# Performance work log

Hardware: AMD Instinct MI355X
Metric: run time of the kernel (lower is better)

Reference implementation:

```python
import jax, jax.numpy as jnp
import numpy as np

NUM_EXPERTS = 32
TOP_K = 4
HIDDEN = 2048
INTER = 768


def setup_inputs() -> dict:
    key = jax.random.key(0)
    k1, k2, k3, k4 = jax.random.split(key, 4)
    hidden_states = jax.random.normal(k1, (4, 512, HIDDEN), dtype=jnp.float32)
    gate = jax.random.normal(k2, (HIDDEN, NUM_EXPERTS), dtype=jnp.float32) * 0.02
    gate_up_proj = jax.random.normal(k3, (NUM_EXPERTS, HIDDEN, 2 * INTER), dtype=jnp.float32) * 0.02
    down_proj = jax.random.normal(k4, (NUM_EXPERTS, INTER, HIDDEN), dtype=jnp.float32) * 0.02
    return {"hidden_states": hidden_states, "gate": gate,
            "gate_up_proj": gate_up_proj, "down_proj": down_proj}


def reference(hidden_states, gate, gate_up_proj, down_proj):
    batch_size = hidden_states.shape[0]
    x = hidden_states.reshape(-1, HIDDEN)  # (T, D)
    num_tokens = x.shape[0]

    # Router
    router_logits = jnp.einsum('TD,DE->TE', x, gate)
    routing_weights = jax.nn.softmax(router_logits.astype(jnp.float32), axis=-1)
    top_k_weights, top_k_indices = jax.lax.top_k(routing_weights, TOP_K)
    top_k_weights = top_k_weights / top_k_weights.sum(axis=-1, keepdims=True)
    top_k_weights = top_k_weights.astype(x.dtype)

    # Scatter top-k weights into full (T, E) matrix
    router_weights = jnp.zeros((num_tokens, NUM_EXPERTS), dtype=x.dtype)
    token_indices = jnp.broadcast_to(jnp.arange(num_tokens)[:, None], top_k_indices.shape)
    router_weights = router_weights.at[token_indices, top_k_indices].set(top_k_weights)

    # Dense all-expert experts pass (faithful to original: computes every expert per token)
    gate_up = jnp.einsum('TD,EDF->TEF', x, gate_up_proj)  # (T, E, 2F)
    g, u = jnp.split(gate_up, 2, axis=-1)
    gated = u * jax.nn.silu(g)  # (T, E, F)
    next_states = jnp.einsum('TEF,EFD->TED', gated, down_proj)
    next_states = (next_states * router_weights[..., None]).sum(axis=1)  # (T, D)
    return next_states.reshape(batch_size, -1, HIDDEN)
```

## Files before the change

kernel.cpp:

```cpp
#include <hip/hip_runtime.h>

#define T_TOKENS 2048
#define HIDDEN   2048
#define NEXPERT  32
#define TOPK     4
#define INTER    768
#define NPAIRS   (T_TOKENS*TOPK)
#define BM       128
#define BK       32
#define MT_MAX   95
#define NT1      24
#define NT2      32
#define NK1      (HIDDEN/BK)
#define NK2      (INTER/BK)

typedef short  bh8 __attribute__((ext_vector_type(8)));
typedef float  fx4 __attribute__((ext_vector_type(4)));

#define AS1 __attribute__((address_space(1)))
#define AS3 __attribute__((address_space(3)))

__device__ __forceinline__ void gload_lds16(const void* g, const void* lds_generic){
    __builtin_amdgcn_global_load_lds(
        (const AS1 void*)(unsigned long long)g,
        (AS3 void*)(unsigned int)(unsigned long long)lds_generic,
        16, 0, 0);
}

__device__ __forceinline__ unsigned int pack2bf(float a, float b){
    unsigned ua = __float_as_uint(a) + 0x8000u;
    unsigned ub = __float_as_uint(b) + 0x8000u;
    return __builtin_amdgcn_perm(ub, ua, 0x07060302u);
}
__device__ __forceinline__ unsigned short f2bfu(float f){
    return (unsigned short)((__float_as_uint(f) + 0x8000u) >> 16);
}

__global__ void cvt_x_k(const float* __restrict__ x, unsigned short* __restrict__ xb){
    int i = (blockIdx.x*256 + threadIdx.x)*8;
    float4 a = *(const float4*)(x+i);
    float4 b = *(const float4*)(x+i+4);
    uint4 o;
    o.x = pack2bf(a.x,a.y); o.y = pack2bf(a.z,a.w);
    o.z = pack2bf(b.x,b.y); o.w = pack2bf(b.z,b.w);
    *(uint4*)(xb+i) = o;
}

__global__ void router_k(const float* __restrict__ x, const float* __restrict__ gate,
                         int* __restrict__ topk_id, float* __restrict__ topk_w,
                         int* __restrict__ counts){
    const int t = blockIdx.x;
    const int l = threadIdx.x;
    const float* xr = x + (size_t)t*HIDDEN;
    float acc[NEXPERT];
#pragma unroll
    for (int e=0;e<NEXPERT;e++) acc[e]=0.f;
    for (int d=l; d<HIDDEN; d+=64){
        float xv = xr[d];
        const float4* g4 = (const float4*)(gate + (size_t)d*NEXPERT);
#pragma unroll
        for (int i=0;i<8;i++){
            float4 g = g4[i];
            acc[i*4+0] += xv*g.x; acc[i*4+1] += xv*g.y;
            acc[i*4+2] += xv*g.z; acc[i*4+3] += xv*g.w;
        }
    }
#pragma unroll
    for (int e=0;e<NEXPERT;e++){
#pragma unroll
        for (int m=1;m<64;m<<=1) acc[e] += __shfl_xor(acc[e], m, 64);
    }
    int ids[TOPK]; float lv[TOPK];
#pragma unroll
    for (int k=0;k<TOPK;k++){
        float m=-1e30f; int mi=0;
#pragma unroll
        for (int e=0;e<NEXPERT;e++){ if (acc[e]>m){ m=acc[e]; mi=e; } }
        ids[k]=mi; lv[k]=m; acc[mi]=-1e30f;
    }
    float ex[TOPK]; float s=0.f;
#pragma unroll
    for (int k=0;k<TOPK;k++){ ex[k]=__expf(lv[k]-lv[0]); s+=ex[k]; }
    if (l==0){
        float inv = 1.f/s;
#pragma unroll
        for (int k=0;k<TOPK;k++){
            topk_id[t*TOPK+k]=ids[k];
            topk_w[t*TOPK+k]=ex[k]*inv;
            atomicAdd(&counts[ids[k]],1);
        }
    }
}

__global__ void sched_k(const int* __restrict__ counts, int* __restrict__ offs,
                        int* __restrict__ cursors, int* __restrict__ nmt,
                        int* __restrict__ te, int* __restrict__ tr0, int* __restrict__ trn){
    if (threadIdx.x==0 && blockIdx.x==0){
        int tot=0, nm=0;
        for (int e=0;e<NEXPERT;e++){
            int c = counts[e];
            offs[e]=tot; cursors[e]=tot;
            for (int s=0;s<c;s+=BM){
                te[nm]=e; tr0[nm]=tot+s; trn[nm]=(c-s)<BM?(c-s):BM; nm++;
            }
            tot+=c;
        }
        *nmt = nm;
    }
}

__global__ void scatter_k(const int* __restrict__ topk_id, const float* __restrict__ topk_w,
                          int* __restrict__ cursors, int* __restrict__ pair_tok,
                          float* __restrict__ pair_w){
    int g = blockIdx.x*256 + threadIdx.x;
    int e = topk_id[g];
    float w = topk_w[g];
    int pos = atomicAdd(&cursors[e],1);
    pair_tok[pos] = g>>2;
    pair_w[pos]  = w;
}

#define TILE_DECODE(NT)                                            \
    const int nwg = gridDim.x;                                     \
    const int q = nwg>>3, r = nwg&7;                               \
    const int xcd = blockIdx.x & 7, bidx = blockIdx.x >> 3;        \
    const int L = (xcd<r ? xcd*(q+1) : r*(q+1)+(xcd-r)*q) + bidx;  \
    const int mt = L % MT_MAX, nt = L / MT_MAX;                    \
    if (mt >= *nmt) return;                                        \
    const int e = te[mt], row0 = tr0[mt], rows = trn[mt];

__global__ __launch_bounds__(256) void gemm1_k(
        const unsigned short* __restrict__ xb, const float* __restrict__ gup,
        const int* __restrict__ nmt, const int* __restrict__ te,
        const int* __restrict__ tr0, const int* __restrict__ trn,
        const int* __restrict__ pair_tok, const float* __restrict__ pair_w,
        unsigned short* __restrict__ gated){
    __shared__ __align__(16) unsigned short As[2][BM*32];
    __shared__ __align__(16) unsigned short Bs[2][64*40];
    __shared__ int   s_tok[BM];
    __shared__ float s_w[BM];

    TILE_DECODE(NT1)
    const int n0 = nt*32;

    const int t = threadIdx.x;
    if (t < BM){
        int p = row0 + t; if (p > NPAIRS-1) p = NPAIRS-1;
        s_tok[t] = pair_tok[p];
        s_w[t]   = pair_w[p];
    }
    __syncthreads();

    const int w = t>>6, lane = t&63;
    const int l15 = lane & 15, kb = lane >> 4;
    const int sA = (l15>>1)&3;

    const int arow0 = w*16 + (lane>>2);
    const int arow1 = 64 + arow0;
    const int ck0 = (lane&3) ^ ((lane>>3)&3);
    const unsigned short* asrc0 = xb + (size_t)s_tok[arow0]*HIDDEN + ck0*8;
    const unsigned short* asrc1 = xb + (size_t)s_tok[arow1]*HIDDEN + ck0*8;

    const int col4 = (t&15)*4;
    const int bd0  = (t>>4)*2;
    const int sB   = (col4>>3)&3;
    const unsigned wb = (unsigned)(col4*80 + (((bd0>>3) ^ sB)<<4) + (bd0&7)*2);
    const int fc = (col4 < 32) ? (n0 + col4) : (736 + n0 + col4);
    const float* bsrc = gup + (size_t)e*HIDDEN*(2*INTER) + (size_t)bd0*(2*INTER) + fc;

    fx4 acc[2][4];
#pragma unroll
    for (int i=0;i<2;i++)
#pragma unroll
        for (int j=0;j<4;j++) acc[i][j] = (fx4)0.f;

    float4 rv0 = *(const float4*)(bsrc);
    float4 rv1 = *(const float4*)(bsrc + 2*INTER);
    gload_lds16(asrc0, &As[0][(w*16)*32]);
    gload_lds16(asrc1, &As[0][(64+w*16)*32]);
    __syncthreads();
    {
        char* bw = (char*)Bs[0];
        *(unsigned*)(bw + wb      ) = pack2bf(rv0.x, rv1.x);
        *(unsigned*)(bw + wb +  80) = pack2bf(rv0.y, rv1.y);
        *(unsigned*)(bw + wb + 160) = pack2bf(rv0.z, rv1.z);
        *(unsigned*)(bw + wb + 240) = pack2bf(rv0.w, rv1.w);
    }
    __syncthreads();

#define G1_STEP(KK, CUR, NXT) do{                                              \
    const int _kn = (KK)+1;                                                    \
    if (_kn < NK1){                                                            \
        const float* _b2 = bsrc + (size_t)_kn*BK*(2*INTER);                    \
        rv0 = *(const float4*)(_b2);                                           \
        rv1 = *(const float4*)(_b2 + 2*INTER);                                 \
        gload_lds16(asrc0 + _kn*BK, &As[NXT][(w*16)*32]);                      \
        gload_lds16(asrc1 + _kn*BK, &As[NXT][(64+w*16)*32]);                   \
    }                                                                          \
    {   const unsigned short* _Ak = As[CUR];                                   \
        const char* _Bk = (const char*)Bs[CUR];                                \
        bh8 _a0 = *(const bh8*)(_Ak + (w*32+l15)*32    + ((kb ^ sA)<<3));      \
        bh8 _a1 = *(const bh8*)(_Ak + (w*32+16+l15)*32 + ((kb ^ sA)<<3));      \
        _Pragma("unroll")                                                      \
        for (int c=0;c<4;c++){                                                 \
            const int bc = c*16 + l15;                                         \
            bh8 _b = *(const bh8*)(_Bk + bc*80 + ((kb ^ ((bc>>3)&3))<<4));     \
            acc[0][c] = __builtin_amdgcn_mfma_f32_16x16x32_bf16(_a0,_b,acc[0][c],0,0,0); \
            acc[1][c] = __builtin_amdgcn_mfma_f32_16x16x32_bf16(_a1,_b,acc[1][c],0,0,0); \
        }                                                                      \
    }                                                                          \
    if (_kn < NK1){                                                            \
        char* _bw = (char*)Bs[NXT];                                            \
        *(unsigned*)(_bw + wb      ) = pack2bf(rv0.x, rv1.x);                  \
        *(unsigned*)(_bw + wb +  80) = pack2bf(rv0.y, rv1.y);                  \
        *(unsigned*)(_bw + wb + 160) = pack2bf(rv0.z, rv1.z);                  \
        *(unsigned*)(_bw + wb + 240) = pack2bf(rv0.w, rv1.w);                  \
    }                                                                          \
    __syncthreads();                                                           \
}while(0)

    for (int k2=0; k2<NK1; k2+=2){
        G1_STEP(k2,   0, 1);
        G1_STEP(k2+1, 1, 0);
    }
#undef G1_STEP

    const int rbase = w*32 + kb*4;
#pragma unroll
    for (int mr=0;mr<2;mr++){
#pragma unroll
        for (int qq=0;qq<4;qq++){
            int row = rbase + mr*16 + qq;
            if (row < rows){
                float wgt = s_w[row];
                size_t prow = (size_t)(row0 + row)*INTER + n0 + l15;
#pragma unroll
                for (int c=0;c<2;c++){
                    float g = acc[mr][c][qq], u = acc[mr][c+2][qq];
                    float sil = g / (1.f + __expf(-g));
                    gated[prow + c*16] = f2bfu(sil*u*wgt);
                }
            }
        }
    }
}

__global__ __launch_bounds__(256) void gemm2_k(
        const unsigned short* __restrict__ gated, const float* __restrict__ down,
        const int* __restrict__ nmt, const int* __restrict__ te,
        const int* __restrict__ tr0, const int* __restrict__ trn,
        const int* __restrict__ pair_tok, float* __restrict__ out){
    __shared__ __align__(16) unsigned short As[2][BM*32];
    __shared__ __align__(16) unsigned short Bs[2][64*40];
    __shared__ int s_tok[BM];

    TILE_DECODE(NT2)
    const int n0 = nt*64;

    const int t = threadIdx.x;
    if (t < BM){
        int p = row0 + t; if (p > NPAIRS-1) p = NPAIRS-1;
        s_tok[t] = pair_tok[p];
    }
    __syncthreads();

    const int w = t>>6, lane = t&63;
    const int l15 = lane & 15, kb = lane >> 4;
    const int sA = (l15>>1)&3;

    const int arow0 = w*16 + (lane>>2);
    const int arow1 = 64 + arow0;
    const int ck0 = (lane&3) ^ ((lane>>3)&3);
    int ap0 = row0 + arow0; if (ap0 > NPAIRS-1) ap0 = NPAIRS-1;
    int ap1 = row0 + arow1; if (ap1 > NPAIRS-1) ap1 = NPAIRS-1;
    const unsigned short* asrc0 = gated + (size_t)ap0*INTER + ck0*8;
    const unsigned short* asrc1 = gated + (size_t)ap1*INTER + ck0*8;

    const int col4 = (t&15)*4;
    const int bd0  = (t>>4)*2;
    const int sB   = (col4>>3)&3;
    const unsigned wb = (unsigned)(col4*80 + (((bd0>>3) ^ sB)<<4) + (bd0&7)*2);
    const float* bsrc = down + (size_t)e*INTER*HIDDEN + (size_t)bd0*HIDDEN + (n0 + col4);

    fx4 acc[2][4];
#pragma unroll
    for (int i=0;i<2;i++)
#pragma unroll
        for (int j=0;j<4;j++) acc[i][j] = (fx4)0.f;

    float4 rv0 = *(const float4*)(bsrc);
    float4 rv1 = *(const float4*)(bsrc + HIDDEN);
    gload_lds16(asrc0, &As[0][(w*16)*32]);
    gload_lds16(asrc1, &As[0][(64+w*16)*32]);
    __syncthreads();
    {
        char* bw = (char*)Bs[0];
        *(unsigned*)(bw + wb      ) = pack2bf(rv0.x, rv1.x);
        *(unsigned*)(bw + wb +  80) = pack2bf(rv0.y, rv1.y);
        *(unsigned*)(bw + wb + 160) = pack2bf(rv0.z, rv1.z);
        *(unsigned*)(bw + wb + 240) = pack2bf(rv0.w, rv1.w);
    }
    __syncthreads();

#define G2_STEP(KK, CUR, NXT) do{                                              \
    const int _kn = (KK)+1;                                                    \
    if (_kn < NK2){                                                            \
        const float* _b2 = bsrc + (size_t)_kn*BK*HIDDEN;                       \
        rv0 = *(const float4*)(_b2);                                           \
        rv1 = *(const float4*)(_b2 + HIDDEN);                                  \
        gload_lds16(asrc0 + _kn*BK, &As[NXT][(w*16)*32]);                      \
        gload_lds16(asrc1 + _kn*BK, &As[NXT][(64+w*16)*32]);                   \
    }                                                                          \
    {   const unsigned short* _Ak = As[CUR];                                   \
        const char* _Bk = (const char*)Bs[CUR];                                \
        bh8 _a0 = *(const bh8*)(_Ak + (w*32+l15)*32    + ((kb ^ sA)<<3));      \
        bh8 _a1 = *(const bh8*)(_Ak + (w*32+16+l15)*32 + ((kb ^ sA)<<3));      \
        _Pragma("unroll")                                                      \
        for (int c=0;c<4;c++){                                                 \
            const int bc = c*16 + l15;                                         \
            bh8 _b = *(const bh8*)(_Bk + bc*80 + ((kb ^ ((bc>>3)&3))<<4));     \
            acc[0][c] = __builtin_amdgcn_mfma_f32_16x16x32_bf16(_a0,_b,acc[0][c],0,0,0); \
            acc[1][c] = __builtin_amdgcn_mfma_f32_16x16x32_bf16(_a1,_b,acc[1][c],0,0,0); \
        }                                                                      \
    }                                                                          \
    if (_kn < NK2){                                                            \
        char* _bw = (char*)Bs[NXT];                                            \
        *(unsigned*)(_bw + wb      ) = pack2bf(rv0.x, rv1.x);                  \
        *(unsigned*)(_bw + wb +  80) = pack2bf(rv0.y, rv1.y);                  \
        *(unsigned*)(_bw + wb + 160) = pack2bf(rv0.z, rv1.z);                  \
        *(unsigned*)(_bw + wb + 240) = pack2bf(rv0.w, rv1.w);                  \
    }                                                                          \
    __syncthreads();                                                           \
}while(0)

    for (int k2=0; k2<NK2; k2+=2){
        G2_STEP(k2,   0, 1);
        G2_STEP(k2+1, 1, 0);
    }
#undef G2_STEP

    const int rbase = w*32 + kb*4;
#pragma unroll
    for (int mr=0;mr<2;mr++){
#pragma unroll
        for (int qq=0;qq<4;qq++){
            int row = rbase + mr*16 + qq;
            if (row < rows){
                float* orow = out + (size_t)s_tok[row]*HIDDEN + n0 + l15;
#pragma unroll
                for (int c=0;c<4;c++)
                    atomicAdd(orow + c*16, acc[mr][c][qq]);
            }
        }
    }
}

extern "C" void kernel_launch(void* const* d_in, const int* in_sizes, int n_in,
                              void* d_out, int out_size, void* d_ws, size_t ws_size,
                              hipStream_t stream){
    const float* x    = (const float*)d_in[0];
    const float* gate = (const float*)d_in[1];
    const float* gup  = (const float*)d_in[2];
    const float* down = (const float*)d_in[3];
    float* out = (float*)d_out;
    char*  ws  = (char*)d_ws;

    int*   topk_id  = (int*)  (ws + 0x00000);
    float* topk_w   = (float*)(ws + 0x08000);
    int*   counts   = (int*)  (ws + 0x10000);
    int*   cursors  = (int*)  (ws + 0x10080);
    int*   offs     = (int*)  (ws + 0x10100);
    int*   nmt      = (int*)  (ws + 0x10180);
    int*   te       = (int*)  (ws + 0x10200);
    int*   tr0      = (int*)  (ws + 0x10400);
    int*   trn      = (int*)  (ws + 0x10600);
    int*   pair_tok = (int*)  (ws + 0x10800);
    float* pair_w   = (float*)(ws + 0x18800);
    unsigned short* gated = (unsigned short*)(ws + 0x21000);
    unsigned short* xb    = (unsigned short*)(ws + 0xC60000);

    hipMemsetAsync(d_out, 0, (size_t)out_size*sizeof(float), stream);
    hipMemsetAsync(counts, 0, NEXPERT*sizeof(int), stream);

    cvt_x_k  <<<T_TOKENS*HIDDEN/(256*8), 256, 0, stream>>>(x, xb);
    router_k <<<T_TOKENS, 64, 0, stream>>>(x, gate, topk_id, topk_w, counts);
    sched_k  <<<1, 64, 0, stream>>>(counts, offs, cursors, nmt, te, tr0, trn);
    scatter_k<<<NPAIRS/256, 256, 0, stream>>>(topk_id, topk_w, cursors, pair_tok, pair_w);
    gemm1_k  <<<MT_MAX*NT1, 256, 0, stream>>>(xb, gup, nmt, te, tr0, trn, pair_tok, pair_w, gated);
    gemm2_k  <<<MT_MAX*NT2, 256, 0, stream>>>(gated, down, nmt, te, tr0, trn, pair_tok, out);
}
```

Baseline: 471.6 us.

## Triple-buffer LDS with prefetch distance two and partial vmcnt waits in both GEMMs

Both expert GEMM kernels move from a double-buffered LDS pipeline to a three-stage ring. The A tile (global_load_lds) and the B registers are prefetched two K-steps ahead, and the full __syncthreads is replaced by explicit s_waitcnt vmcnt(4)/lgkmcnt(0) plus s_barrier. The aim is to hide global load latency behind MFMA work and to stop waiting on loads that are still in flight. It costs 50% more LDS per block, which may lower occupancy. The hand-counted vmcnt values are fragile, and clamping the prefetch index at the tail issues redundant loads.

```diff
diff --git a/kernel.cpp b/kernel.cpp
--- a/kernel.cpp
+++ b/kernel.cpp
@@ -129,14 +129,44 @@
     if (mt >= *nmt) return;                                        \
     const int e = te[mt], row0 = tr0[mt], rows = trn[mt];
 
+#define GSTEP(KK, NK, BSTR, C0, C1, C2, RL0, RL1, RW0, RW1) do{                 \
+    int _ks = (KK)+2; if (_ks > (NK)-1) _ks = (NK)-1;                           \
+    const float* _bp = bsrc + (size_t)_ks*BK*(BSTR);                            \
+    RL0 = *(const float4*)(_bp);                                                \
+    RL1 = *(const float4*)(_bp + (BSTR));                                       \
+    gload_lds16(asrc0 + _ks*BK, &As[C2][(w*16)*32]);                            \
+    gload_lds16(asrc1 + _ks*BK, &As[C2][(64+w*16)*32]);                         \
+    {   const unsigned short* _Ak = As[C0];                                     \
+        const char* _Bk = (const char*)Bs[C0];                                  \
+        bh8 _a0 = *(const bh8*)(_Ak + (w*32+l15)*32    + ((kb^sA)<<3));         \
+        bh8 _a1 = *(const bh8*)(_Ak + (w*32+16+l15)*32 + ((kb^sA)<<3));         \
+        _Pragma("unroll")                                                       \
+        for (int c=0;c<4;c++){                                                  \
+            const int bc = c*16 + l15;                                          \
+            bh8 _b = *(const bh8*)(_Bk + bc*80 + ((kb ^ ((bc>>3)&3))<<4));      \
+            acc[0][c] = __builtin_amdgcn_mfma_f32_16x16x32_bf16(_a0,_b,acc[0][c],0,0,0); \
+            acc[1][c] = __builtin_amdgcn_mfma_f32_16x16x32_bf16(_a1,_b,acc[1][c],0,0,0); \
+        }                                                                       \
+    }                                                                           \
+    asm volatile("s_waitcnt vmcnt(4)" ::: "memory");                            \
+    {   char* _bw = (char*)Bs[C1];                                              \
+        *(unsigned*)(_bw + wb      ) = pack2bf(RW0.x, RW1.x);                   \
+        *(unsigned*)(_bw + wb +  80) = pack2bf(RW0.y, RW1.y);                   \
+        *(unsigned*)(_bw + wb + 160) = pack2bf(RW0.z, RW1.z);                   \
+        *(unsigned*)(_bw + wb + 240) = pack2bf(RW0.w, RW1.w);                   \
+    }                                                                           \
+    asm volatile("s_waitcnt lgkmcnt(0)" ::: "memory");                          \
+    __builtin_amdgcn_s_barrier();                                               \
+}while(0)
+
 __global__ __launch_bounds__(256) void gemm1_k(
         const unsigned short* __restrict__ xb, const float* __restrict__ gup,
         const int* __restrict__ nmt, const int* __restrict__ te,
         const int* __restrict__ tr0, const int* __restrict__ trn,
         const int* __restrict__ pair_tok, const float* __restrict__ pair_w,
         unsigned short* __restrict__ gated){
-    __shared__ __align__(16) unsigned short As[2][BM*32];
-    __shared__ __align__(16) unsigned short Bs[2][64*40];
+    __shared__ __align__(16) unsigned short As[3][BM*32];
+    __shared__ __align__(16) unsigned short Bs[3][64*40];
     __shared__ int   s_tok[BM];
     __shared__ float s_w[BM];
 
@@ -174,56 +204,35 @@
 #pragma unroll
         for (int j=0;j<4;j++) acc[i][j] = (fx4)0.f;
 
-    float4 rv0 = *(const float4*)(bsrc);
-    float4 rv1 = *(const float4*)(bsrc + 2*INTER);
-    gload_lds16(asrc0, &As[0][(w*16)*32]);
-    gload_lds16(asrc1, &As[0][(64+w*16)*32]);
-    __syncthreads();
+    float4 rE0, rE1, rO0, rO1;
+    gload_lds16(asrc0,      &As[0][(w*16)*32]);
+    gload_lds16(asrc1,      &As[0][(64+w*16)*32]);
+    gload_lds16(asrc0 + BK, &As[1][(w*16)*32]);
+    gload_lds16(asrc1 + BK, &As[1][(64+w*16)*32]);
+    rE0 = *(const float4*)(bsrc);
+    rE1 = *(const float4*)(bsrc + 2*INTER);
+    rO0 = *(const float4*)(bsrc + (size_t)BK*2*INTER);
+    rO1 = *(const float4*)(bsrc + (size_t)BK*2*INTER + 2*INTER);
+    asm volatile("s_waitcnt vmcnt(0)" ::: "memory");
     {
-        char* bw = (char*)Bs[0];
-        *(unsigned*)(bw + wb      ) = pack2bf(rv0.x, rv1.x);
-        *(unsigned*)(bw + wb +  80) = pack2bf(rv0.y, rv1.y);
-        *(unsigned*)(bw + wb + 160) = pack2bf(rv0.z, rv1.z);
-        *(unsigned*)(bw + wb + 240) = pack2bf(rv0.w, rv1.w);
-    }
-    __syncthreads();
-
-#define G1_STEP(KK, CUR, NXT) do{                                              \
-    const int _kn = (KK)+1;                                                    \
-    if (_kn < NK1){                                                            \
-        const float* _b2 = bsrc + (size_t)_kn*BK*(2*INTER);                    \
-        rv0 = *(const float4*)(_b2);                                           \
-        rv1 = *(const float4*)(_b2 + 2*INTER);                                 \
-        gload_lds16(asrc0 + _kn*BK, &As[NXT][(w*16)*32]);                      \
-        gload_lds16(asrc1 + _kn*BK, &As[NXT][(64+w*16)*32]);                   \
-    }                                                                          \
-    {   const unsigned short* _Ak = As[CUR];                                   \
-        const char* _Bk = (const char*)Bs[CUR];                                \
-        bh8 _a0 = *(const bh8*)(_Ak + (w*32+l15)*32    + ((kb ^ sA)<<3));      \
-        bh8 _a1 = *(const bh8*)(_Ak + (w*32+16+l15)*32 + ((kb ^ sA)<<3));      \
-        _Pragma("unroll")                                                      \
-        for (int c=0;c<4;c++){                                                 \
-            const int bc = c*16 + l15;                                         \
-            bh8 _b = *(const bh8*)(_Bk + bc*80 + ((kb ^ ((bc>>3)&3))<<4));     \
-            acc[0][c] = __builtin_amdgcn_mfma_f32_16x16x32_bf16(_a0,_b,acc[0][c],0,0,0); \
-            acc[1][c] = __builtin_amdgcn_mfma_f32_16x16x32_bf16(_a1,_b,acc[1][c],0,0,0); \
-        }                                                                      \
-    }                                                                          \
-    if (_kn < NK1){                                                            \
-        char* _bw = (char*)Bs[NXT];                                            \
-        *(unsigned*)(_bw + wb      ) = pack2bf(rv0.x, rv1.x);                  \
-        *(unsigned*)(_bw + wb +  80) = pack2bf(rv0.y, rv1.y);                  \
-        *(unsigned*)(_bw + wb + 160) = pack2bf(rv0.z, rv1.z);                  \
-        *(unsigned*)(_bw + wb + 240) = pack2bf(rv0.w, rv1.w);                  \
-    }                                                                          \
-    __syncthreads();                                                           \
-}while(0)
-
-    for (int k2=0; k2<NK1; k2+=2){
-        G1_STEP(k2,   0, 1);
-        G1_STEP(k2+1, 1, 0);
-    }
-#undef G1_STEP
+        char* bw0 = (char*)Bs[0];
+        *(unsigned*)(bw0 + wb      ) = pack2bf(rE0.x, rE1.x);
+        *(unsigned*)(bw0 + wb +  80) = pack2bf(rE0.y, rE1.y);
+        *(unsigned*)(bw0 + wb + 160) = pack2bf(rE0.z, rE1.z);
+        *(unsigned*)(bw0 + wb + 240) = pack2bf(rE0.w, rE1.w);
+    }
+    asm volatile("s_waitcnt lgkmcnt(0)" ::: "memory");
+    __builtin_amdgcn_s_barrier();
+
+    int c0 = 0;
+    for (int k2 = 0; k2 < NK1; k2 += 2){
+        int c1 = c0+1; if (c1==3) c1 = 0;
+        int c2 = c1+1; if (c2==3) c2 = 0;
+        GSTEP(k2,   NK1, 2*INTER, c0, c1, c2, rE0, rE1, rO0, rO1);
+        GSTEP(k2+1, NK1, 2*INTER, c1, c2, c0, rO0, rO1, rE0, rE1);
+        c0 = c2;
+    }
+    asm volatile("s_waitcnt vmcnt(0)" ::: "memory");
 
     const int rbase = w*32 + kb*4;
 #pragma unroll
@@ -250,8 +259,8 @@
         const int* __restrict__ nmt, const int* __restrict__ te,
         const int* __restrict__ tr0, const int* __restrict__ trn,
         const int* __restrict__ pair_tok, float* __restrict__ out){
-    __shared__ __align__(16) unsigned short As[2][BM*32];
-    __shared__ __align__(16) unsigned short Bs[2][64*40];
+    __shared__ __align__(16) unsigned short As[3][BM*32];
+    __shared__ __align__(16) unsigned short Bs[3][64*40];
     __shared__ int s_tok[BM];
 
     TILE_DECODE(NT2)
@@ -288,56 +297,35 @@
 #pragma unroll
         for (int j=0;j<4;j++) acc[i][j] = (fx4)0.f;
 
-    float4 rv0 = *(const float4*)(bsrc);
-    float4 rv1 = *(const float4*)(bsrc + HIDDEN);
-    gload_lds16(asrc0, &As[0][(w*16)*32]);
-    gload_lds16(asrc1, &As[0][(64+w*16)*32]);
-    __syncthreads();
+    float4 rE0, rE1, rO0, rO1;
+    gload_lds16(asrc0,      &As[0][(w*16)*32]);
+    gload_lds16(asrc1,      &As[0][(64+w*16)*32]);
+    gload_lds16(asrc0 + BK, &As[1][(w*16)*32]);
+    gload_lds16(asrc1 + BK, &As[1][(64+w*16)*32]);
+    rE0 = *(const float4*)(bsrc);
+    rE1 = *(const float4*)(bsrc + HIDDEN);
+    rO0 = *(const float4*)(bsrc + (size_t)BK*HIDDEN);
+    rO1 = *(const float4*)(bsrc + (size_t)BK*HIDDEN + HIDDEN);
+    asm volatile("s_waitcnt vmcnt(0)" ::: "memory");
     {
-        char* bw = (char*)Bs[0];
-        *(unsigned*)(bw + wb      ) = pack2bf(rv0.x, rv1.x);
-        *(unsigned*)(bw + wb +  80) = pack2bf(rv0.y, rv1.y);
-        *(unsigned*)(bw + wb + 160) = pack2bf(rv0.z, rv1.z);
-        *(unsigned*)(bw + wb + 240) = pack2bf(rv0.w, rv1.w);
-    }
-    __syncthreads();
-
-#define G2_STEP(KK, CUR, NXT) do{                                              \
-    const int _kn = (KK)+1;                                                    \
-    if (_kn < NK2){                                                            \
-        const float* _b2 = bsrc + (size_t)_kn*BK*HIDDEN;                       \
-        rv0 = *(const float4*)(_b2);                                           \
-        rv1 = *(const float4*)(_b2 + HIDDEN);                                  \
-        gload_lds16(asrc0 + _kn*BK, &As[NXT][(w*16)*32]);                      \
-        gload_lds16(asrc1 + _kn*BK, &As[NXT][(64+w*16)*32]);                   \
-    }                                                                          \
-    {   const unsigned short* _Ak = As[CUR];                                   \
-        const char* _Bk = (const char*)Bs[CUR];                                \
-        bh8 _a0 = *(const bh8*)(_Ak + (w*32+l15)*32    + ((kb ^ sA)<<3));      \
-        bh8 _a1 = *(const bh8*)(_Ak + (w*32+16+l15)*32 + ((kb ^ sA)<<3));      \
-        _Pragma("unroll")                                                      \
-        for (int c=0;c<4;c++){                                                 \
-            const int bc = c*16 + l15;                                         \
-            bh8 _b = *(const bh8*)(_Bk + bc*80 + ((kb ^ ((bc>>3)&3))<<4));     \
-            acc[0][c] = __builtin_amdgcn_mfma_f32_16x16x32_bf16(_a0,_b,acc[0][c],0,0,0); \
-            acc[1][c] = __builtin_amdgcn_mfma_f32_16x16x32_bf16(_a1,_b,acc[1][c],0,0,0); \
-        }                                                                      \
-    }                                                                          \
-    if (_kn < NK2){                                                            \
-        char* _bw = (char*)Bs[NXT];                                            \
-        *(unsigned*)(_bw + wb      ) = pack2bf(rv0.x, rv1.x);                  \
-        *(unsigned*)(_bw + wb +  80) = pack2bf(rv0.y, rv1.y);                  \
-        *(unsigned*)(_bw + wb + 160) = pack2bf(rv0.z, rv1.z);                  \
-        *(unsigned*)(_bw + wb + 240) = pack2bf(rv0.w, rv1.w);                  \
-    }                                                                          \
-    __syncthreads();                                                           \
-}while(0)
-
-    for (int k2=0; k2<NK2; k2+=2){
-        G2_STEP(k2,   0, 1);
-        G2_STEP(k2+1, 1, 0);
-    }
-#undef G2_STEP
+        char* bw0 = (char*)Bs[0];
+        *(unsigned*)(bw0 + wb      ) = pack2bf(rE0.x, rE1.x);
+        *(unsigned*)(bw0 + wb +  80) = pack2bf(rE0.y, rE1.y);
+        *(unsigned*)(bw0 + wb + 160) = pack2bf(rE0.z, rE1.z);
+        *(unsigned*)(bw0 + wb + 240) = pack2bf(rE0.w, rE1.w);
+    }
+    asm volatile("s_waitcnt lgkmcnt(0)" ::: "memory");
+    __builtin_amdgcn_s_barrier();
+
+    int c0 = 0;
+    for (int k2 = 0; k2 < NK2; k2 += 2){
+        int c1 = c0+1; if (c1==3) c1 = 0;
+        int c2 = c1+1; if (c2==3) c2 = 0;
+        GSTEP(k2,   NK2, HIDDEN, c0, c1, c2, rE0, rE1, rO0, rO1);
+        GSTEP(k2+1, NK2, HIDDEN, c1, c2, c0, rO0, rO1, rE0, rE1);
+        c0 = c2;
+    }
+    asm volatile("s_waitcnt vmcnt(0)" ::: "memory");
 
     const int rbase = w*32 + kb*4;
 #pragma unroll
```

Result: no change. 477.2 us (+1.2%).
